# Kernel optimization log

Measured on AMD Instinct MI355X. Metric: run time of the kernel, lower is better.

The kernel has to match this reference:

```python
import jax, jax.numpy as jnp
import numpy as np

SNUM = 8           # number of select-PUF stages
PUF_LEN = 64       # arbiter PUF length -> phi dim = PUF_LEN + 1
BATCH = 262144     # number of challenge-response pairs
D = 2 ** SNUM      # 256 combinations


def _make_kron_tables():
    """Replicates the W/B kron construction from combineMPUF.__init__.
    Returns Wmat, Bmat of shape [SNUM, D]; row i is W[i]/B[i] (originally [1, D])."""
    tmpX = np.array([[1], [1]])
    Ws, Bs = [], []
    for i in range(SNUM):
        w = np.array([[-1], [1]])
        b = np.array([[1], [0]])
        for _ in range(i + 1, SNUM):
            w = np.kron(tmpX, w)
            b = np.kron(tmpX, b)
        for _ in range(i):
            w = np.kron(w, tmpX)
            b = np.kron(b, tmpX)
        Ws.append(w.T[0])
        Bs.append(b.T[0])
    return (jnp.asarray(np.stack(Ws), jnp.float32),
            jnp.asarray(np.stack(Bs), jnp.float32))


def setup_inputs() -> dict:
    key = jax.random.key(0)
    k_phi, k_ws, k_bs, k_wd, k_bd = jax.random.split(key, 5)
    F = PUF_LEN + 1
    scale = 1.0 / np.sqrt(F)  # ~ torch Linear init scale
    phi = jax.random.normal(k_phi, (BATCH, F), dtype=jnp.float32)
    W_S = jax.random.uniform(k_ws, (SNUM, F), jnp.float32, -scale, scale)
    b_S = jax.random.uniform(k_bs, (SNUM,), jnp.float32, -scale, scale)
    W_D = jax.random.uniform(k_wd, (D, F), jnp.float32, -scale, scale)
    b_D = jax.random.uniform(k_bd, (D,), jnp.float32, -scale, scale)
    Wmat, Bmat = _make_kron_tables()
    return {"phi": phi, "W_S": W_S, "b_S": b_S, "W_D": W_D, "b_D": b_D,
            "Wmat": Wmat, "Bmat": Bmat}


def reference(phi, W_S, b_S, W_D, b_D, Wmat, Bmat):
    # phi: [B, F]; W_S: [SNUM, F]; W_D: [D, F]; Wmat/Bmat: [SNUM, D]
    Sdelta = phi @ W_S.T + b_S            # [B, SNUM]
    Ddelta = phi @ W_D.T + b_D            # [B, D]
    Souts = jax.nn.sigmoid(Sdelta)        # [B, SNUM]
    Douts = jax.nn.sigmoid(Ddelta)        # [B, D]
    # sigmoid-gated outer-product chain: M = prod_i (s_i * w_i + b_i)
    M = jnp.ones_like(Douts)
    for i in range(SNUM):                 # small fixed structural loop
        M = M * (Souts[:, i:i + 1] * Wmat[i] + Bmat[i])
    ans = jnp.sum(Douts * M * 0.99999, axis=-1, keepdims=True)  # [B, 1]
    reliability_output = jnp.abs(Sdelta)  # [B, SNUM]
    return ans, reliability_output
```

## Files before the change

kernel.cpp:

```cpp
#include <hip/hip_runtime.h>

typedef float  f32x4  __attribute__((ext_vector_type(4)));
typedef float  f32x4a __attribute__((ext_vector_type(4), aligned(4)));
typedef float  f32x2  __attribute__((ext_vector_type(2)));
typedef __bf16 bf16x8 __attribute__((ext_vector_type(8)));
typedef short  short8 __attribute__((ext_vector_type(8)));

#define F      65
#define NTT    17
#define KS3    3
#define RPB    128
#define NCHUNK (NTT*KS3*64)

__device__ __forceinline__ unsigned short f2bf(float f) {
  unsigned int u = __builtin_bit_cast(unsigned int, f);
  u += 0x7FFFu + ((u >> 16) & 1u);
  return (unsigned short)(u >> 16);
}
__device__ __forceinline__ float fast_sigmoid(float x) {
  float e = __builtin_amdgcn_exp2f(-1.4426950408889634f * x);
  return __builtin_amdgcn_rcpf(1.0f + e);
}
template<int CTRL>
__device__ __forceinline__ float dpp_mov(float v) {
  return __builtin_bit_cast(float,
    __builtin_amdgcn_update_dpp(0, __builtin_bit_cast(int, v), CTRL, 0xF, 0xF, true));
}

__global__ void prep_w(const float* __restrict__ W_S, const float* __restrict__ b_S,
                       const float* __restrict__ W_D, const float* __restrict__ b_D,
                       unsigned short* __restrict__ wsb) {
  int b = blockIdx.x;
  int t = b / 3, s = b % 3;
  int l = threadIdx.x;
  int c = l & 15, q = l >> 4;
  short8 out;
#pragma unroll
  for (int j = 0; j < 8; ++j) {
    int k = 32 * s + 8 * q + j;
    float v = 0.0f;
    if (t < 16) {
      int n = 16 * t + c;
      if (k < F)       v = W_D[n * F + k];
      else if (k == F) v = b_D[n];
    } else if (c < 8) {
      if (k < F)       v = W_S[c * F + k];
      else if (k == F) v = b_S[c];
    }
    out[j] = (short)f2bf(v);
  }
  reinterpret_cast<short8*>(wsb)[b * 64 + l] = out;
}

__launch_bounds__(512, 4)
__global__ void mpuf_main(const float* __restrict__ phi,
                          const unsigned short* __restrict__ wsb,
                          float* __restrict__ out_ans,
                          float* __restrict__ out_rel) {
  __shared__ short8 ldsB[NCHUNK];
  __shared__ float  soutv[RPB][10];
  __shared__ float  rowrec[RPB][18];

  const int tid  = threadIdx.x;
  const int wave = tid >> 6;
  const int l    = tid & 63;
  const int c    = l & 15;
  const int q    = l >> 4;
  const int wrow = wave * 16;
  const int brow = blockIdx.x * RPB;

  const float* prow = phi + (size_t)(brow + wrow + c) * F;

  f32x4a f4[4];
#pragma unroll
  for (int s = 0; s < 2; ++s) {
    f4[2 * s]     = *reinterpret_cast<const f32x4a*>(prow + 32 * s + 8 * q);
    f4[2 * s + 1] = *reinterpret_cast<const f32x4a*>(prow + 32 * s + 8 * q + 4);
  }
  const float a64 = prow[64];

  const short8* wsv = reinterpret_cast<const short8*>(wsb);
#pragma unroll
  for (int i = 0; i < 7; ++i) {
    int idx = tid + i * 512;
    if (idx < NCHUNK) ldsB[idx] = wsv[idx];
  }

  bf16x8 af[3];
#pragma unroll
  for (int s = 0; s < 2; ++s) {
    short8 ar;
#pragma unroll
    for (int j = 0; j < 4; ++j) {
      ar[j]     = (short)f2bf(f4[2 * s][j]);
      ar[j + 4] = (short)f2bf(f4[2 * s + 1][j]);
    }
    af[s] = __builtin_bit_cast(bf16x8, ar);
  }
  {
    short8 ar = {0, 0, 0, 0, 0, 0, 0, 0};
    if (q == 0) {
      ar[0] = (short)f2bf(a64);
      ar[1] = (short)0x3F80;
    }
    af[2] = __builtin_bit_cast(bf16x8, ar);
  }

  __syncthreads();

  f32x4 accS = {};
#pragma unroll
  for (int s = 0; s < KS3; ++s)
    accS = __builtin_amdgcn_mfma_f32_16x16x32_bf16(
               af[s], __builtin_bit_cast(bf16x8, ldsB[(16 * KS3 + s) * 64 + l]),
               accS, 0, 0, 0);

  if (c < 8) {
#pragma unroll
    for (int r = 0; r < 4; ++r) {
      const int R = wrow + q * 4 + r;
      float sd = accS[r];
      out_rel[(size_t)(brow + R) * 8 + c] = fabsf(sd);
      soutv[R][c] = fast_sigmoid(sd);
    }
  }

  float Ml[4];
#pragma unroll
  for (int r = 0; r < 4; ++r) {
    const int R = wrow + q * 4 + r;
    f32x2 p01 = *reinterpret_cast<const f32x2*>(&soutv[R][0]);
    f32x2 p23 = *reinterpret_cast<const f32x2*>(&soutv[R][2]);
    f32x2 p45 = *reinterpret_cast<const f32x2*>(&soutv[R][4]);
    f32x2 p67 = *reinterpret_cast<const f32x2*>(&soutv[R][6]);
    float m = 0.99999f;
    m *= (c & 1) ? p01[0] : 1.0f - p01[0];
    m *= (c & 2) ? p01[1] : 1.0f - p01[1];
    m *= (c & 4) ? p23[0] : 1.0f - p23[0];
    m *= (c & 8) ? p23[1] : 1.0f - p23[1];
    Ml[r] = m;
    float mt = (c & 1) ? p45[0] : 1.0f - p45[0];
    mt *= (c & 2) ? p45[1] : 1.0f - p45[1];
    mt *= (c & 4) ? p67[0] : 1.0f - p67[0];
    mt *= (c & 8) ? p67[1] : 1.0f - p67[1];
    rowrec[R][c] = mt;
  }

  float ansacc[4] = {0.0f, 0.0f, 0.0f, 0.0f};

#pragma unroll 1
  for (int tp = 0; tp < 8; ++tp) {
    const int t0 = 2 * tp, t1 = t0 + 1;
    f32x4 A0 = {}, A1 = {};
#pragma unroll
    for (int s = 0; s < KS3; ++s)
      A0 = __builtin_amdgcn_mfma_f32_16x16x32_bf16(
               af[s], __builtin_bit_cast(bf16x8, ldsB[(t0 * KS3 + s) * 64 + l]),
               A0, 0, 0, 0);
#pragma unroll
    for (int s = 0; s < KS3; ++s)
      A1 = __builtin_amdgcn_mfma_f32_16x16x32_bf16(
               af[s], __builtin_bit_cast(bf16x8, ldsB[(t1 * KS3 + s) * 64 + l]),
               A1, 0, 0, 0);
#pragma unroll
    for (int r = 0; r < 4; ++r) {
      const int R = wrow + q * 4 + r;
      f32x2 w = *reinterpret_cast<const f32x2*>(&rowrec[R][t0]);
      float d0 = fast_sigmoid(A0[r]);
      float d1 = fast_sigmoid(A1[r]);
      ansacc[r] = fmaf(d0, Ml[r] * w[0], ansacc[r]);
      ansacc[r] = fmaf(d1, Ml[r] * w[1], ansacc[r]);
    }
  }

#pragma unroll
  for (int r = 0; r < 4; ++r) {
    float v = ansacc[r];
    v += dpp_mov<0xB1>(v);
    v += dpp_mov<0x4E>(v);
    v += dpp_mov<0x141>(v);
    v += dpp_mov<0x140>(v);
    ansacc[r] = v;
  }
  if (c == 0) {
    f32x4 o = { ansacc[0], ansacc[1], ansacc[2], ansacc[3] };
    *reinterpret_cast<f32x4*>(&out_ans[brow + wrow + q * 4]) = o;
  }
}

extern "C" void kernel_launch(void* const* d_in, const int* in_sizes, int n_in,
                              void* d_out, int out_size, void* d_ws, size_t ws_size,
                              hipStream_t stream) {
  const float* phi = (const float*)d_in[0];
  const float* W_S = (const float*)d_in[1];
  const float* b_S = (const float*)d_in[2];
  const float* W_D = (const float*)d_in[3];
  const float* b_D = (const float*)d_in[4];
  const int rows = in_sizes[0] / F;
  unsigned short* wsb = (unsigned short*)d_ws;
  float* out_ans = (float*)d_out;
  float* out_rel = out_ans + rows;
  hipLaunchKernelGGL(prep_w, dim3(NTT * KS3), dim3(64), 0, stream,
                     W_S, b_S, W_D, b_D, wsb);
  hipLaunchKernelGGL(mpuf_main, dim3(rows / RPB), dim3(512), 0, stream,
                     phi, wsb, out_ans, out_rel);
}
```

Baseline: 40.47 us.

## Prescale W_D by -log2e, factor Ml out of loop, use 1024-thread blocks

Folds the -log2(e) factor into the bf16 W_D weights at prep time, so the inner sigmoid skips a multiply. Pulls the per-row Ml factor out of the tile loop so it is applied once before the reduction. Fully unrolls the 16-tile loop and doubles the block to 1024 threads (256 rows), which spreads the shared-weight LDS fill over more rows. The larger block may lower occupancy and raise register pressure, and the bf16 casts now use the compiler's conversion instead of manual rounding.

```diff
diff --git a/kernel.cpp b/kernel.cpp
--- a/kernel.cpp
+++ b/kernel.cpp
@@ -2,29 +2,35 @@
 
 typedef float  f32x4  __attribute__((ext_vector_type(4)));
 typedef float  f32x4a __attribute__((ext_vector_type(4), aligned(4)));
-typedef float  f32x2  __attribute__((ext_vector_type(2)));
+typedef float  f32x2a __attribute__((ext_vector_type(2), aligned(4)));
 typedef __bf16 bf16x8 __attribute__((ext_vector_type(8)));
 typedef short  short8 __attribute__((ext_vector_type(8)));
 
 #define F      65
 #define NTT    17
 #define KS3    3
-#define RPB    128
+#define RPB    256
 #define NCHUNK (NTT*KS3*64)
+#define NEGL2E -1.4426950408889634f
 
-__device__ __forceinline__ unsigned short f2bf(float f) {
-  unsigned int u = __builtin_bit_cast(unsigned int, f);
-  u += 0x7FFFu + ((u >> 16) & 1u);
-  return (unsigned short)(u >> 16);
+__device__ __forceinline__ float fast_sigmoid(float x) {
+  float e = __builtin_amdgcn_exp2f(NEGL2E * x);
+  return __builtin_amdgcn_rcpf(1.0f + e);
 }
-__device__ __forceinline__ float fast_sigmoid(float x) {
-  float e = __builtin_amdgcn_exp2f(-1.4426950408889634f * x);
-  return __builtin_amdgcn_rcpf(1.0f + e);
+__device__ __forceinline__ float sig_prescaled(float a) {
+  return __builtin_amdgcn_rcpf(1.0f + __builtin_amdgcn_exp2f(a));
 }
 template<int CTRL>
 __device__ __forceinline__ float dpp_mov(float v) {
   return __builtin_bit_cast(float,
     __builtin_amdgcn_update_dpp(0, __builtin_bit_cast(int, v), CTRL, 0xF, 0xF, true));
+}
+__device__ __forceinline__ float reduce16(float v) {
+  v += dpp_mov<0xB1>(v);
+  v += dpp_mov<0x4E>(v);
+  v += dpp_mov<0x141>(v);
+  v += dpp_mov<0x140>(v);
+  return v;
 }
 
 __global__ void prep_w(const float* __restrict__ W_S, const float* __restrict__ b_S,
@@ -41,25 +47,27 @@
     float v = 0.0f;
     if (t < 16) {
       int n = 16 * t + c;
-      if (k < F)       v = W_D[n * F + k];
-      else if (k == F) v = b_D[n];
+      if (k < F)       v = NEGL2E * W_D[n * F + k];
+      else if (k == F) v = NEGL2E * b_D[n];
     } else if (c < 8) {
       if (k < F)       v = W_S[c * F + k];
       else if (k == F) v = b_S[c];
     }
-    out[j] = (short)f2bf(v);
+    unsigned int u = __builtin_bit_cast(unsigned int, v);
+    u += 0x7FFFu + ((u >> 16) & 1u);
+    out[j] = (short)(u >> 16);
   }
   reinterpret_cast<short8*>(wsb)[b * 64 + l] = out;
 }
 
-__launch_bounds__(512, 4)
+__launch_bounds__(1024, 8)
 __global__ void mpuf_main(const float* __restrict__ phi,
                           const unsigned short* __restrict__ wsb,
                           float* __restrict__ out_ans,
                           float* __restrict__ out_rel) {
   __shared__ short8 ldsB[NCHUNK];
   __shared__ float  soutv[RPB][10];
-  __shared__ float  rowrec[RPB][18];
+  __shared__ float  mtrec[RPB][17];
 
   const int tid  = threadIdx.x;
   const int wave = tid >> 6;
@@ -81,47 +89,42 @@
 
   const short8* wsv = reinterpret_cast<const short8*>(wsb);
 #pragma unroll
-  for (int i = 0; i < 7; ++i) {
-    int idx = tid + i * 512;
+  for (int i = 0; i < 4; ++i) {
+    int idx = tid + i * 1024;
     if (idx < NCHUNK) ldsB[idx] = wsv[idx];
   }
 
   bf16x8 af[3];
 #pragma unroll
   for (int s = 0; s < 2; ++s) {
-    short8 ar;
+    bf16x8 v;
 #pragma unroll
     for (int j = 0; j < 4; ++j) {
-      ar[j]     = (short)f2bf(f4[2 * s][j]);
-      ar[j + 4] = (short)f2bf(f4[2 * s + 1][j]);
+      v[j]     = (__bf16)f4[s * 2][j];
+      v[j + 4] = (__bf16)f4[s * 2 + 1][j];
     }
-    af[s] = __builtin_bit_cast(bf16x8, ar);
+    af[s] = v;
   }
   {
-    short8 ar = {0, 0, 0, 0, 0, 0, 0, 0};
-    if (q == 0) {
-      ar[0] = (short)f2bf(a64);
-      ar[1] = (short)0x3F80;
-    }
-    af[2] = __builtin_bit_cast(bf16x8, ar);
+    bf16x8 v = {};
+    if (q == 0) { v[0] = (__bf16)a64; v[1] = (__bf16)1.0f; }
+    af[2] = v;
   }
 
   __syncthreads();
 
-  f32x4 accS = {};
+  f32x4 aS = {};
 #pragma unroll
-  for (int s = 0; s < KS3; ++s)
-    accS = __builtin_amdgcn_mfma_f32_16x16x32_bf16(
-               af[s], __builtin_bit_cast(bf16x8, ldsB[(16 * KS3 + s) * 64 + l]),
-               accS, 0, 0, 0);
-
+  for (int s = 0; s < KS3; ++s) {
+    bf16x8 b = __builtin_bit_cast(bf16x8, ldsB[(16 * KS3 + s) * 64 + l]);
+    aS = __builtin_amdgcn_mfma_f32_16x16x32_bf16(af[s], b, aS, 0, 0, 0);
+  }
   if (c < 8) {
 #pragma unroll
     for (int r = 0; r < 4; ++r) {
       const int R = wrow + q * 4 + r;
-      float sd = accS[r];
-      out_rel[(size_t)(brow + R) * 8 + c] = fabsf(sd);
-      soutv[R][c] = fast_sigmoid(sd);
+      out_rel[(size_t)(brow + R) * 8 + c] = fabsf(aS[r]);
+      soutv[R][c] = fast_sigmoid(aS[r]);
     }
   }
 
@@ -129,10 +132,10 @@
 #pragma unroll
   for (int r = 0; r < 4; ++r) {
     const int R = wrow + q * 4 + r;
-    f32x2 p01 = *reinterpret_cast<const f32x2*>(&soutv[R][0]);
-    f32x2 p23 = *reinterpret_cast<const f32x2*>(&soutv[R][2]);
-    f32x2 p45 = *reinterpret_cast<const f32x2*>(&soutv[R][4]);
-    f32x2 p67 = *reinterpret_cast<const f32x2*>(&soutv[R][6]);
+    f32x2a p01 = *reinterpret_cast<const f32x2a*>(&soutv[R][0]);
+    f32x2a p23 = *reinterpret_cast<const f32x2a*>(&soutv[R][2]);
+    f32x2a p45 = *reinterpret_cast<const f32x2a*>(&soutv[R][4]);
+    f32x2a p67 = *reinterpret_cast<const f32x2a*>(&soutv[R][6]);
     float m = 0.99999f;
     m *= (c & 1) ? p01[0] : 1.0f - p01[0];
     m *= (c & 2) ? p01[1] : 1.0f - p01[1];
@@ -143,47 +146,30 @@
     mt *= (c & 2) ? p45[1] : 1.0f - p45[1];
     mt *= (c & 4) ? p67[0] : 1.0f - p67[0];
     mt *= (c & 8) ? p67[1] : 1.0f - p67[1];
-    rowrec[R][c] = mt;
+    mtrec[R][c] = mt;
   }
 
-  float ansacc[4] = {0.0f, 0.0f, 0.0f, 0.0f};
+  float ans[4] = {0, 0, 0, 0};
 
-#pragma unroll 1
-  for (int tp = 0; tp < 8; ++tp) {
-    const int t0 = 2 * tp, t1 = t0 + 1;
-    f32x4 A0 = {}, A1 = {};
 #pragma unroll
-    for (int s = 0; s < KS3; ++s)
-      A0 = __builtin_amdgcn_mfma_f32_16x16x32_bf16(
-               af[s], __builtin_bit_cast(bf16x8, ldsB[(t0 * KS3 + s) * 64 + l]),
-               A0, 0, 0, 0);
+  for (int t = 0; t < 16; ++t) {
+    f32x4 A = {};
 #pragma unroll
-    for (int s = 0; s < KS3; ++s)
-      A1 = __builtin_amdgcn_mfma_f32_16x16x32_bf16(
-               af[s], __builtin_bit_cast(bf16x8, ldsB[(t1 * KS3 + s) * 64 + l]),
-               A1, 0, 0, 0);
+    for (int s = 0; s < KS3; ++s) {
+      bf16x8 b = __builtin_bit_cast(bf16x8, ldsB[(t * KS3 + s) * 64 + l]);
+      A = __builtin_amdgcn_mfma_f32_16x16x32_bf16(af[s], b, A, 0, 0, 0);
+    }
 #pragma unroll
     for (int r = 0; r < 4; ++r) {
       const int R = wrow + q * 4 + r;
-      f32x2 w = *reinterpret_cast<const f32x2*>(&rowrec[R][t0]);
-      float d0 = fast_sigmoid(A0[r]);
-      float d1 = fast_sigmoid(A1[r]);
-      ansacc[r] = fmaf(d0, Ml[r] * w[0], ansacc[r]);
-      ansacc[r] = fmaf(d1, Ml[r] * w[1], ansacc[r]);
+      ans[r] = fmaf(sig_prescaled(A[r]), mtrec[R][t], ans[r]);
     }
   }
 
 #pragma unroll
-  for (int r = 0; r < 4; ++r) {
-    float v = ansacc[r];
-    v += dpp_mov<0xB1>(v);
-    v += dpp_mov<0x4E>(v);
-    v += dpp_mov<0x141>(v);
-    v += dpp_mov<0x140>(v);
-    ansacc[r] = v;
-  }
+  for (int r = 0; r < 4; ++r) ans[r] = reduce16(Ml[r] * ans[r]);
   if (c == 0) {
-    f32x4 o = { ansacc[0], ansacc[1], ansacc[2], ansacc[3] };
+    f32x4 o = { ans[0], ans[1], ans[2], ans[3] };
     *reinterpret_cast<f32x4*>(&out_ans[brow + wrow + q * 4]) = o;
   }
 }
@@ -202,6 +188,6 @@
   float* out_rel = out_ans + rows;
   hipLaunchKernelGGL(prep_w, dim3(NTT * KS3), dim3(64), 0, stream,
                      W_S, b_S, W_D, b_D, wsb);
-  hipLaunchKernelGGL(mpuf_main, dim3(rows / RPB), dim3(512), 0, stream,
+  hipLaunchKernelGGL(mpuf_main, dim3(rows / RPB), dim3(1024), 0, stream,
                      phi, wsb, out_ans, out_rel);
 }
```

New measurement: 59.98 us. 1.48x slower.
